# Kernel optimization log

Measured on AMD Instinct MI355X. Metric: run time of the kernel, lower is better.

The kernel has to match this reference:

```python
import jax, jax.numpy as jnp
import numpy as np

BANDWIDTH = 0.1
N_STEPS = 5
TOL = 1e-3
BASE = 3
COORD_OFFSET = 512   # bins assumed within (-512, 511] per dim
COORD_BITS = 10      # 3 dims * 10 bits = 30 bits, fits int32


def _generate_offsets(d, base=3):
    # replicates torch.meshgrid(indexing='ij') over arange(-1, base-1)
    ranges = [np.arange(-1, base - 1) for _ in range(d)]
    mesh = np.meshgrid(*ranges, indexing='ij')
    return jnp.asarray(np.stack(mesh, axis=-1).reshape(-1, d), dtype=jnp.int32)


def _pack_keys(bins):
    # bins: (..., d) int32 -> unique scalar int32 key per bin coordinate
    d = bins.shape[-1]
    key = jnp.zeros(bins.shape[:-1], dtype=jnp.int32)
    for k in range(d):  # tiny fixed loop over dims
        key = (key << COORD_BITS) | (bins[..., k] + COORD_OFFSET)
    return key


def _step(X, offsets, bandwidth):
    # One mean-shift step: bin points, scatter-add sums/counts over the
    # union of offset-shifted bins (torch.unique replaced by exact key
    # packing + sort-based grouping, fixed shapes for jit).
    n, d = X.shape
    m = offsets.shape[0]  # base ** d
    bins = (X / bandwidth).astype(jnp.int32)          # trunc-toward-zero == torch .int()
    shifted = bins[:, None, :] + offsets[None, :, :]  # (n, m, d)
    keys = _pack_keys(shifted).reshape(-1)            # (n*m,)
    K = keys.shape[0]

    order = jnp.argsort(keys)
    skeys = keys[order]
    new_grp = jnp.concatenate(
        [jnp.zeros((1,), jnp.int32), (skeys[1:] != skeys[:-1]).astype(jnp.int32)]
    )
    seg = jnp.cumsum(new_grp)                         # group id per sorted position

    # X repeated once per offset (matches X.repeat(1, m).reshape(-1, d))
    Xflat = jnp.broadcast_to(X[:, None, :], (n, m, d)).reshape(-1, d)
    sum_per = jax.ops.segment_sum(Xflat[order], seg, num_segments=K)          # (K, d)
    cnt_per = jax.ops.segment_sum(jnp.ones((K,), X.dtype), seg, num_segments=K)

    # segment id per original (unsorted) flat position == inverse_indices
    seg_orig = jnp.zeros((K,), seg.dtype).at[order].set(seg)
    sum_mapped = sum_per[seg_orig].reshape(n, m, d).sum(axis=1)   # (n, d)
    cnt_mapped = cnt_per[seg_orig].reshape(n, m).sum(axis=1)      # (n,)
    return sum_mapped / cnt_mapped[:, None]


def setup_inputs() -> dict:
    key = jax.random.key(0)
    X = jax.random.normal(key, (200000, 3), dtype=jnp.float32)
    return {"X": X}


def reference(X):
    n, d = X.shape
    offsets = _generate_offsets(d, BASE)

    def body(carry, _):
        Xc, done = carry
        Xn = _step(Xc, offsets, BANDWIDTH)
        Xn = jnp.where(done, Xc, Xn)  # freeze once converged (== early break)
        conv = jnp.max(jnp.linalg.norm(Xn - Xc, axis=1)) <= TOL
        return (Xn, done | conv), None

    (Xout, _), _ = jax.lax.scan(body, (X, jnp.array(False)), None, length=N_STEPS)
    return Xout
```

## Files before the change

kernel.cpp:

```cpp
#include <hip/hip_runtime.h>


constexpr float BW   = 0.1f;
constexpr float TOL2 = 1e-6f;
constexpr int DIM  = 112, OFF = 56;
constexpr int DIM2 = DIM * DIM;
constexpr int CELLS = DIM * DIM * DIM;
constexpr int CLW = CELLS / 32;
constexpr int RDIM = 16, RC = 7;
constexpr int NREG = RDIM * RDIM * RDIM;
constexpr int RC3 = RC * RC * RC;
constexpr int NB_A = 128, BLK = 256;
constexpr int NF = 2048;
constexpr int IPB = 51;
constexpr float FPS = 16777216.0f;
constexpr double FPSI = 1.0 / 16777216.0;

typedef float vf2 __attribute__((ext_vector_type(2)));

__device__ __forceinline__ int clampb(int v) { return v < 0 ? 0 : (v > DIM - 1 ? DIM - 1 : v); }
__device__ __forceinline__ int binf(float v) { return clampb((int)(v / BW) + OFF); }
__device__ __forceinline__ int flatb(int bx, int by, int bz) { return (bx * DIM + by) * DIM + bz; }
__device__ __forceinline__ int regOf(int bx, int by, int bz) {
    return ((bx / RC) * RDIM + (by / RC)) * RDIM + (bz / RC);
}
__device__ __forceinline__ int lcOf(int bx, int by, int bz) {
    return ((bx % RC) * RC + (by % RC)) * RC + (bz % RC);
}

__device__ __forceinline__ void pk_add(float* p, float a, float b) {
#if defined(__has_builtin) && __has_builtin(__builtin_amdgcn_global_atomic_fadd_v2f32)
    vf2 v = {a, b};
    __builtin_amdgcn_global_atomic_fadd_v2f32((vf2*)p, v);
#else
    atomicAdd(p, a);
    atomicAdd(p + 1, b);
#endif
}

__launch_bounds__(BLK)
__global__ void k_histA(const float* __restrict__ X, int n, int* __restrict__ blockHist,
                        float4* __restrict__ zeroA, float4* __restrict__ zeroB) {
    __shared__ int h[NREG];
    for (int i = threadIdx.x; i < NREG; i += blockDim.x) h[i] = 0;
    __syncthreads();
    int stride = gridDim.x * blockDim.x;
    for (int i = blockIdx.x * blockDim.x + threadIdx.x; i < n; i += stride) {
        float x = X[3 * i + 0], y = X[3 * i + 1], z = X[3 * i + 2];
        atomicAdd(&h[regOf(binf(x), binf(y), binf(z))], 1);
    }
    __syncthreads();
    for (int i = threadIdx.x; i < NREG; i += blockDim.x)
        blockHist[blockIdx.x * NREG + i] = h[i];
    for (int i = blockIdx.x * blockDim.x + threadIdx.x; i < CELLS; i += stride) {
        zeroA[i] = make_float4(0.f, 0.f, 0.f, 0.f);
        zeroB[i] = make_float4(0.f, 0.f, 0.f, 0.f);
    }
}

__global__ void k_colscan(int* __restrict__ blockHist, int* __restrict__ regionPS) {
    int r = blockIdx.x * blockDim.x + threadIdx.x;
    if (r >= NREG) return;
    int run = 0;
    for (int b = 0; b < NB_A; ++b) {
        int idx = b * NREG + r;
        int v = blockHist[idx];
        blockHist[idx] = run;
        run += v;
    }
    regionPS[r] = run;
}

__launch_bounds__(1024)
__global__ void k_regprefix(int* __restrict__ regionPS) {
    __shared__ int buf[1024];
    int t = threadIdx.x;
    int v0 = regionPS[4 * t + 0], v1 = regionPS[4 * t + 1];
    int v2 = regionPS[4 * t + 2], v3 = regionPS[4 * t + 3];
    int s = v0 + v1 + v2 + v3;
    buf[t] = s;
    __syncthreads();
    for (int d = 1; d < 1024; d <<= 1) {
        int add = (t >= d) ? buf[t - d] : 0;
        __syncthreads();
        buf[t] += add;
        __syncthreads();
    }
    int excl = buf[t] - s;
    regionPS[4 * t + 0] = excl;
    regionPS[4 * t + 1] = excl + v0;
    regionPS[4 * t + 2] = excl + v0 + v1;
    regionPS[4 * t + 3] = excl + v0 + v1 + v2;
    if (t == 1023) regionPS[4096] = buf[1023];
}

__launch_bounds__(BLK)
__global__ void k_scatterA(const float* __restrict__ X, int n,
                           const int* __restrict__ blockHist,
                           const int* __restrict__ regionPS,
                           float4* __restrict__ bucket, float4* __restrict__ zeroC) {
    __shared__ int cur[NREG];
    for (int i = threadIdx.x; i < NREG; i += blockDim.x) cur[i] = 0;
    __syncthreads();
    int stride = gridDim.x * blockDim.x;
    for (int i = blockIdx.x * blockDim.x + threadIdx.x; i < n; i += stride) {
        float x = X[3 * i + 0], y = X[3 * i + 1], z = X[3 * i + 2];
        int r = regOf(binf(x), binf(y), binf(z));
        int pos = regionPS[r] + blockHist[blockIdx.x * NREG + r] + atomicAdd(&cur[r], 1);
        bucket[pos] = make_float4(x, y, z, __int_as_float(i));
    }
    for (int i = blockIdx.x * blockDim.x + threadIdx.x; i < CELLS; i += stride)
        zeroC[i] = make_float4(0.f, 0.f, 0.f, 0.f);
}

__launch_bounds__(BLK)
__global__ void k_binB(const float4* __restrict__ bucket, const int* __restrict__ regionPS,
                       float4* __restrict__ A, int* __restrict__ E0,
                       int* __restrict__ PIdx, int* __restrict__ gM0) {
    __shared__ unsigned long long aX[RC3], aY[RC3], aZ[RC3];
    __shared__ unsigned aC[RC3];
    __shared__ int cidx[RC3];
    __shared__ int cnt, cur, sBase;
    int r = blockIdx.x;
    for (int c = threadIdx.x; c < RC3; c += blockDim.x) {
        aX[c] = 0ull; aY[c] = 0ull; aZ[c] = 0ull; aC[c] = 0u;
    }
    if (threadIdx.x == 0) { cnt = 0; cur = 0; }
    __syncthreads();
    int start = regionPS[r], end = regionPS[r + 1];
    for (int i = start + threadIdx.x; i < end; i += blockDim.x) {
        float4 p = bucket[i];
        int lc = lcOf(binf(p.x), binf(p.y), binf(p.z));
        atomicAdd(&aX[lc], (unsigned long long)(long long)rintf(p.x * FPS));
        atomicAdd(&aY[lc], (unsigned long long)(long long)rintf(p.y * FPS));
        atomicAdd(&aZ[lc], (unsigned long long)(long long)rintf(p.z * FPS));
        atomicAdd(&aC[lc], 1u);
    }
    __syncthreads();
    int myc = 0;
    for (int c = threadIdx.x; c < RC3; c += blockDim.x)
        if (aC[c] > 0u) ++myc;
    if (myc) atomicAdd(&cnt, myc);
    __syncthreads();
    if (threadIdx.x == 0 && cnt > 0) sBase = atomicAdd(gM0, cnt);
    __syncthreads();
    int rx = r / (RDIM * RDIM), ry = (r / RDIM) % RDIM, rz = r % RDIM;
    for (int c = threadIdx.x; c < RC3; c += blockDim.x) {
        if (aC[c] > 0u) {
            int idx = sBase + atomicAdd(&cur, 1);
            cidx[c] = idx;
            int bx = rx * RC + c / (RC * RC);
            int by = ry * RC + (c / RC) % RC;
            int bz = rz * RC + c % RC;
            int b = flatb(bx, by, bz);
            E0[idx] = b;
            A[b] = make_float4((float)((double)(long long)aX[c] * FPSI),
                               (float)((double)(long long)aY[c] * FPSI),
                               (float)((double)(long long)aZ[c] * FPSI),
                               (float)aC[c]);
        }
    }
    __syncthreads();
    for (int i = start + threadIdx.x; i < end; i += blockDim.x) {
        float4 p = bucket[i];
        int lc = lcOf(binf(p.x), binf(p.y), binf(p.z));
        PIdx[__float_as_int(p.w)] = cidx[lc];
    }
}

__launch_bounds__(BLK)
__global__ void k_fused(
    const float4* __restrict__ src, const int* __restrict__ list, const int* __restrict__ pK,
    float4* __restrict__ REo, int* __restrict__ IDXo, float4* __restrict__ eposInit,
    float4* __restrict__ tgt, unsigned* __restrict__ clT,
    int updS, const float* __restrict__ X, int n, const int* __restrict__ PIdx,
    const float4* __restrict__ REp, const int* __restrict__ IDXp,
    const int* __restrict__ pM0, float4* __restrict__ epos,
    unsigned* __restrict__ notConv,
    const int* __restrict__ clearList, const int* __restrict__ pKc,
    float4* __restrict__ clearGrid, int chkMask, int lastStep) {
    __shared__ float4 sh[BLK];
    __shared__ float shW[IPB];
    __shared__ unsigned sFlag;
    if (threadIdx.x == 0) sFlag = 0;
    __syncthreads();
    int K = *pK;
    int NC = (K + IPB - 1) / IPB;
    int BC = NC;
    if (BC > NF - 256) BC = NF - 256;
    const float t5[5] = {1.f, 2.f, 3.f, 2.f, 1.f};
    bool moved = false;

    if ((int)blockIdx.x < BC) {
        bool frozen = false;
        if (chkMask) {
            #pragma unroll
            for (int t = 1; t <= 4; ++t)
                if ((chkMask >> t) & 1) frozen |= (notConv[t] == 0u);
        }
        if (!frozen) {
        int first, last, step;
        if (BC >= 64) {
            int xcd = blockIdx.x & 7, loc = blockIdx.x >> 3;
            int cpx = (NC + 7) >> 3;
            int bpx = ((BC - 1 - xcd) >> 3) + 1;
            first = xcd * cpx + loc;
            last = (xcd + 1) * cpx; if (last > NC) last = NC;
            step = bpx;
        } else {
            first = blockIdx.x; last = NC; step = BC;
        }
        for (int ib = first; ib < last; ib += step) {
            int li = threadIdx.x / 5;
            int dx = threadIdx.x % 5;
            int item = ib * IPB + li;
            float4 part = make_float4(0.f, 0.f, 0.f, 0.f);
            if (li < IPB && item < K) {
                int b = list[item];
                int bx = b / DIM2, rem = b % DIM2;
                int by = rem / DIM, bz = rem % DIM;
                if (dx == 2) shW[li] = src[b].w;
                int ix = bx + dx - 2;
                if ((unsigned)ix < (unsigned)DIM) {
                    float wx = t5[dx];
                    if (by >= 2 && by <= DIM - 3 && bz >= 2 && bz <= DIM - 3) {
                        #pragma unroll
                        for (int dy = 0; dy < 5; ++dy) {
                            float wxy = wx * t5[dy];
                            const float4* row = src + flatb(ix, by + dy - 2, bz - 2);
                            #pragma unroll
                            for (int dz = 0; dz < 5; ++dz) {
                                float w = wxy * t5[dz];
                                float4 e = row[dz];
                                part.x = fmaf(w, e.x, part.x);
                                part.y = fmaf(w, e.y, part.y);
                                part.z = fmaf(w, e.z, part.z);
                                part.w = fmaf(w, e.w, part.w);
                            }
                        }
                    } else {
                        for (int dy = 0; dy < 5; ++dy) {
                            int iy = by + dy - 2;
                            if ((unsigned)iy >= (unsigned)DIM) continue;
                            float wxy = wx * t5[dy];
                            for (int dz = 0; dz < 5; ++dz) {
                                int iz = bz + dz - 2;
                                if ((unsigned)iz >= (unsigned)DIM) continue;
                                float w = wxy * t5[dz];
                                float4 e = src[flatb(ix, iy, iz)];
                                part.x = fmaf(w, e.x, part.x);
                                part.y = fmaf(w, e.y, part.y);
                                part.z = fmaf(w, e.z, part.z);
                                part.w = fmaf(w, e.w, part.w);
                            }
                        }
                    }
                }
            }
            sh[threadIdx.x] = part;
            __syncthreads();
            if (threadIdx.x < 64) {
                int item2 = ib * IPB + threadIdx.x;
                bool valid = (threadIdx.x < IPB) && (item2 < K);
                int bn = -1;
                float4 sv = make_float4(0.f, 0.f, 0.f, 0.f);
                if (valid) {
                    int base5 = threadIdx.x * 5;
                    float4 a0 = sh[base5 + 0], a1 = sh[base5 + 1], a2 = sh[base5 + 2];
                    float4 a3 = sh[base5 + 3], a4 = sh[base5 + 4];
                    float sx = a0.x + a1.x + a2.x + a3.x + a4.x;
                    float sy = a0.y + a1.y + a2.y + a3.y + a4.y;
                    float sz = a0.z + a1.z + a2.z + a3.z + a4.z;
                    float sc = a0.w + a1.w + a2.w + a3.w + a4.w;
                    int b = list[item2];
                    float W = shW[threadIdx.x];
                    float4 np = make_float4(sx / sc, sy / sc, sz / sc, W);
                    REo[item2] = np;
                    IDXo[b] = item2;
                    if (eposInit) eposInit[item2] = np;
                    if (!lastStep) {
                        bn = flatb(binf(np.x), binf(np.y), binf(np.z));
                        sv = make_float4(W * np.x, W * np.y, W * np.z, W);
                    }
                }
                if (!lastStep) {
                    int pbn = __shfl_up(bn, 1, 64);
                    unsigned f = (threadIdx.x == 0 || pbn != bn) ? 1u : 0u;
                    unsigned nf = __shfl_down(f, 1, 64);
                    bool leader = valid && (threadIdx.x == 63 || nf != 0u);
                    #pragma unroll
                    for (int off = 1; off < 64; off <<= 1) {
                        float ox = __shfl_up(sv.x, off, 64);
                        float oy = __shfl_up(sv.y, off, 64);
                        float oz = __shfl_up(sv.z, off, 64);
                        float ow = __shfl_up(sv.w, off, 64);
                        unsigned of = __shfl_up(f, off, 64);
                        if ((int)threadIdx.x >= off) {
                            if (!f) { sv.x += ox; sv.y += oy; sv.z += oz; sv.w += ow; }
                            f |= of;
                        }
                    }
                    if (leader) {
                        float* cell = (float*)&tgt[bn];
                        pk_add(cell + 0, sv.x, sv.y);
                        pk_add(cell + 2, sv.z, sv.w);
                        atomicOr(&clT[(unsigned)bn >> 5], 1u << (bn & 31));
                    }
                }
            }
            __syncthreads();
        }
        }
    } else {
        int U = (updS > 0) ? (X ? n : *pM0) : 0;
        int CL = clearList ? *pKc : 0;
        int total = U + CL;
        bool done = false;
        if (updS > 1) {
            for (int t = 1; t < updS; ++t) done |= (notConv[t] == 0u);
        }
        int stride = (NF - BC) * blockDim.x;
        for (int idx = (blockIdx.x - BC) * blockDim.x + threadIdx.x; idx < total;
             idx += stride) {
            if (idx < U) {
                int e = idx;
                if (X) {
                    float x = X[3 * e + 0], y = X[3 * e + 1], z = X[3 * e + 2];
                    float4 rr = REp[PIdx[e]];
                    float ex = rr.x - x, ey = rr.y - y, ez = rr.z - z;
                    moved |= (fmaf(ex, ex, fmaf(ey, ey, ez * ez)) > TOL2);
                } else if (!done) {
                    float4 p = epos[e];
                    int j = IDXp[flatb(binf(p.x), binf(p.y), binf(p.z))];
                    float4 rr = REp[j];
                    float ex = rr.x - p.x, ey = rr.y - p.y, ez = rr.z - p.z;
                    moved |= (fmaf(ex, ex, fmaf(ey, ey, ez * ez)) > TOL2);
                    epos[e] = make_float4(rr.x, rr.y, rr.z, p.w);
                }
            } else {
                clearGrid[clearList[idx - U]] = make_float4(0.f, 0.f, 0.f, 0.f);
            }
        }
    }
    if (moved) sFlag = 1;
    __syncthreads();
    if (threadIdx.x == 0 && updS > 0 && sFlag) notConv[updS] = 1u;
}

__launch_bounds__(BLK)
__global__ void k_compactM(unsigned* __restrict__ mask, int* __restrict__ listOut,
                           int* __restrict__ pKout) {
    __shared__ int scan[BLK];
    __shared__ int sBase;
    int i = blockIdx.x * blockDim.x + threadIdx.x;
    unsigned w = (i < CLW) ? mask[i] : 0u;
    if (i < CLW && w) mask[i] = 0u;
    int c = __popc(w);
    scan[threadIdx.x] = c;
    __syncthreads();
    for (int d = 1; d < BLK; d <<= 1) {
        int add = (threadIdx.x >= (unsigned)d) ? scan[threadIdx.x - d] : 0;
        __syncthreads();
        scan[threadIdx.x] += add;
        __syncthreads();
    }
    if (threadIdx.x == BLK - 1) {
        int tot = scan[BLK - 1];
        sBase = tot ? atomicAdd(pKout, tot) : 0;
    }
    __syncthreads();
    int base = sBase + scan[threadIdx.x] - c;
    int bb = i * 32;
    while (w) {
        int b = __ffs(w) - 1;
        listOut[base++] = bb + b;
        w &= w - 1;
    }
}

__launch_bounds__(BLK)
__global__ void k_fin(const float4* __restrict__ REa, const int* __restrict__ IDXa,
                      const float4* __restrict__ epos, const int* __restrict__ pM0,
                      const unsigned* __restrict__ notConv, float4* __restrict__ fpos) {
    int M0 = *pM0;
    bool done = false;
    for (int t = 1; t <= 4; ++t) done |= (notConv[t] == 0u);
    for (int e = blockIdx.x * blockDim.x + threadIdx.x; e < M0;
         e += gridDim.x * blockDim.x) {
        float4 p = epos[e];
        if (!done) {
            float4 rr = REa[IDXa[flatb(binf(p.x), binf(p.y), binf(p.z))]];
            p.x = rr.x; p.y = rr.y; p.z = rr.z;
        }
        fpos[e] = p;
    }
}

__global__ void k_map(const int* __restrict__ PIdx, int n, const float4* __restrict__ fpos,
                      float* __restrict__ out) {
    int i = blockIdx.x * blockDim.x + threadIdx.x;
    if (i >= n) return;
    float4 p = fpos[PIdx[i]];
    out[3 * i + 0] = p.x;
    out[3 * i + 1] = p.y;
    out[3 * i + 2] = p.z;
}

extern "C" void kernel_launch(void* const* d_in, const int* in_sizes, int n_in,
                              void* d_out, int out_size, void* d_ws, size_t ws_size,
                              hipStream_t stream) {
    const float* X = (const float*)d_in[0];
    int n = in_sizes[0] / 3;

    char* ws = (char*)d_ws;
    int*      cnt     = (int*)ws;
    unsigned* notConv = (unsigned*)(ws + 32);
    size_t mB = (size_t)CLW * 4;
    size_t gB = (size_t)CELLS * 16;
    unsigned* m0 = (unsigned*)(ws + 256);
    unsigned* m1 = (unsigned*)(ws + 256 + mB);
    float4* A = (float4*)(ws + 256 + 2 * mB);
    float4* B = (float4*)((char*)A + gB);
    float4* C = (float4*)((char*)B + gB);
    int* IDXa = (int*)((char*)C + gB);
    int* IDXb = IDXa + CELLS;
    float4* REa  = (float4*)(IDXb + CELLS);
    float4* REb  = REa + n;
    float4* epos = REb + n;
    int* E0   = (int*)(epos + n);
    int* La   = E0 + n;
    int* Lb   = La + n;
    int* Lc   = Lb + n;
    int* Ld   = Lc + n;
    int* PIdx = Ld + n;
    float4* bucket = (float4*)(PIdx + n);
    int* blockHist = (int*)(bucket + n);
    int* regionPS  = blockHist + NB_A * NREG;

    hipMemsetAsync(ws, 0, 256 + 2 * mB, stream);

    const int NCM = (CLW + BLK - 1) / BLK;

    k_histA<<<NB_A, BLK, 0, stream>>>(X, n, blockHist, A, B);
    k_colscan<<<NREG / BLK, BLK, 0, stream>>>(blockHist, regionPS);
    k_regprefix<<<1, 1024, 0, stream>>>(regionPS);
    k_scatterA<<<NB_A, BLK, 0, stream>>>(X, n, blockHist, regionPS, bucket, C);
    k_binB<<<NREG, BLK, 0, stream>>>(bucket, regionPS, A, E0, PIdx, &cnt[1]);

    k_fused<<<NF, BLK, 0, stream>>>(A, E0, &cnt[1], REa, IDXa, epos,
                                    B, m0,
                                    0, nullptr, n, nullptr, nullptr, nullptr, nullptr,
                                    nullptr, notConv, nullptr, nullptr, nullptr, 0, 0);
    k_compactM<<<NCM, BLK, 0, stream>>>(m0, La, &cnt[2]);
    k_fused<<<NF, BLK, 0, stream>>>(B, La, &cnt[2], REb, IDXb, nullptr,
                                    C, m1,
                                    1, X, n, PIdx, REa, IDXa, &cnt[1], nullptr,
                                    notConv, E0, &cnt[1], A, 0, 0);
    k_compactM<<<NCM, BLK, 0, stream>>>(m1, Lb, &cnt[3]);
    k_fused<<<NF, BLK, 0, stream>>>(C, Lb, &cnt[3], REa, IDXa, nullptr,
                                    A, m0,
                                    2, nullptr, n, nullptr, REb, IDXb, &cnt[1], epos,
                                    notConv, La, &cnt[2], B, 0b00010, 0);
    k_compactM<<<NCM, BLK, 0, stream>>>(m0, Lc, &cnt[4]);
    k_fused<<<NF, BLK, 0, stream>>>(A, Lc, &cnt[4], REb, IDXb, nullptr,
                                    B, m1,
                                    3, nullptr, n, nullptr, REa, IDXa, &cnt[1], epos,
                                    notConv, nullptr, nullptr, nullptr, 0b00110, 0);
    k_compactM<<<NCM, BLK, 0, stream>>>(m1, Ld, &cnt[5]);
    k_fused<<<NF, BLK, 0, stream>>>(B, Ld, &cnt[5], REa, IDXa, nullptr,
                                    nullptr, nullptr,
                                    4, nullptr, n, nullptr, REb, IDXb, &cnt[1], epos,
                                    notConv, nullptr, nullptr, nullptr, 0b01110, 1);

    k_fin<<<256, BLK, 0, stream>>>(REa, IDXa, epos, &cnt[1], notConv, REb);
    k_map<<<(n + BLK - 1) / BLK, BLK, 0, stream>>>(PIdx, n, REb, (float*)d_out);
}
```

Before: 246.8 us.

## Gather stencil neighbors through compact index grid instead of dense float4 grid

The dense float4 grid reads in the 5x5x5 stencil are replaced by reads of an int index grid. Each index is validated against the compact list, and only then is the neighbor's float4 loaded from a compacted array. The compaction kernel now also writes that index grid and copies the grid values into the compact array. The goal is to cut memory traffic from mostly-empty cells, at the cost of an extra dependent load per neighbor and divergent validation branches. The stale-index validation also replaces the old grid clearing for some steps, and changes which buffers are cleared.

```diff
diff --git a/kernel.cpp b/kernel.cpp
--- a/kernel.cpp
+++ b/kernel.cpp
@@ -115,7 +115,8 @@
 
 __launch_bounds__(BLK)
 __global__ void k_binB(const float4* __restrict__ bucket, const int* __restrict__ regionPS,
-                       float4* __restrict__ A, int* __restrict__ E0,
+                       float4* __restrict__ AC, int* __restrict__ E0,
+                       int* __restrict__ IDXa,
                        int* __restrict__ PIdx, int* __restrict__ gM0) {
     __shared__ unsigned long long aX[RC3], aY[RC3], aZ[RC3];
     __shared__ unsigned aC[RC3];
@@ -154,10 +155,11 @@
             int bz = rz * RC + c % RC;
             int b = flatb(bx, by, bz);
             E0[idx] = b;
-            A[b] = make_float4((float)((double)(long long)aX[c] * FPSI),
-                               (float)((double)(long long)aY[c] * FPSI),
-                               (float)((double)(long long)aZ[c] * FPSI),
-                               (float)aC[c]);
+            IDXa[b] = idx;
+            AC[idx] = make_float4((float)((double)(long long)aX[c] * FPSI),
+                                  (float)((double)(long long)aY[c] * FPSI),
+                                  (float)((double)(long long)aZ[c] * FPSI),
+                                  (float)aC[c]);
         }
     }
     __syncthreads();
@@ -170,8 +172,9 @@
 
 __launch_bounds__(BLK)
 __global__ void k_fused(
-    const float4* __restrict__ src, const int* __restrict__ list, const int* __restrict__ pK,
-    float4* __restrict__ REo, int* __restrict__ IDXo, float4* __restrict__ eposInit,
+    const float4* __restrict__ AC, const int* __restrict__ list, const int* __restrict__ pK,
+    const int* __restrict__ IDXsrc,
+    float4* __restrict__ REo, float4* __restrict__ eposInit,
     float4* __restrict__ tgt, unsigned* __restrict__ clT,
     int updS, const float* __restrict__ X, int n, const int* __restrict__ PIdx,
     const float4* __restrict__ REp, const int* __restrict__ IDXp,
@@ -180,7 +183,6 @@
     const int* __restrict__ clearList, const int* __restrict__ pKc,
     float4* __restrict__ clearGrid, int chkMask, int lastStep) {
     __shared__ float4 sh[BLK];
-    __shared__ float shW[IPB];
     __shared__ unsigned sFlag;
     if (threadIdx.x == 0) sFlag = 0;
     __syncthreads();
@@ -219,23 +221,34 @@
                 int b = list[item];
                 int bx = b / DIM2, rem = b % DIM2;
                 int by = rem / DIM, bz = rem % DIM;
-                if (dx == 2) shW[li] = src[b].w;
                 int ix = bx + dx - 2;
                 if ((unsigned)ix < (unsigned)DIM) {
                     float wx = t5[dx];
                     if (by >= 2 && by <= DIM - 3 && bz >= 2 && bz <= DIM - 3) {
+                        int idxv[25];
+                        #pragma unroll
+                        for (int dy = 0; dy < 5; ++dy) {
+                            const int* gr = IDXsrc + flatb(ix, by + dy - 2, bz - 2);
+                            #pragma unroll
+                            for (int dz = 0; dz < 5; ++dz)
+                                idxv[dy * 5 + dz] = gr[dz];
+                        }
+                        int rowb = flatb(ix, by - 2, bz - 2);
                         #pragma unroll
                         for (int dy = 0; dy < 5; ++dy) {
                             float wxy = wx * t5[dy];
-                            const float4* row = src + flatb(ix, by + dy - 2, bz - 2);
                             #pragma unroll
                             for (int dz = 0; dz < 5; ++dz) {
-                                float w = wxy * t5[dz];
-                                float4 e = row[dz];
-                                part.x = fmaf(w, e.x, part.x);
-                                part.y = fmaf(w, e.y, part.y);
-                                part.z = fmaf(w, e.z, part.z);
-                                part.w = fmaf(w, e.w, part.w);
+                                int id = idxv[dy * 5 + dz];
+                                if ((unsigned)id < (unsigned)K &&
+                                    list[id] == rowb + dy * DIM + dz) {
+                                    float4 e = AC[id];
+                                    float w = wxy * t5[dz];
+                                    part.x = fmaf(w, e.x, part.x);
+                                    part.y = fmaf(w, e.y, part.y);
+                                    part.z = fmaf(w, e.z, part.z);
+                                    part.w = fmaf(w, e.w, part.w);
+                                }
                             }
                         }
                     } else {
@@ -246,12 +259,16 @@
                             for (int dz = 0; dz < 5; ++dz) {
                                 int iz = bz + dz - 2;
                                 if ((unsigned)iz >= (unsigned)DIM) continue;
-                                float w = wxy * t5[dz];
-                                float4 e = src[flatb(ix, iy, iz)];
-                                part.x = fmaf(w, e.x, part.x);
-                                part.y = fmaf(w, e.y, part.y);
-                                part.z = fmaf(w, e.z, part.z);
-                                part.w = fmaf(w, e.w, part.w);
+                                int cell = flatb(ix, iy, iz);
+                                int id = IDXsrc[cell];
+                                if ((unsigned)id < (unsigned)K && list[id] == cell) {
+                                    float4 e = AC[id];
+                                    float w = wxy * t5[dz];
+                                    part.x = fmaf(w, e.x, part.x);
+                                    part.y = fmaf(w, e.y, part.y);
+                                    part.z = fmaf(w, e.z, part.z);
+                                    part.w = fmaf(w, e.w, part.w);
+                                }
                             }
                         }
                     }
@@ -272,11 +289,9 @@
                     float sy = a0.y + a1.y + a2.y + a3.y + a4.y;
                     float sz = a0.z + a1.z + a2.z + a3.z + a4.z;
                     float sc = a0.w + a1.w + a2.w + a3.w + a4.w;
-                    int b = list[item2];
-                    float W = shW[threadIdx.x];
+                    float W = AC[item2].w;
                     float4 np = make_float4(sx / sc, sy / sc, sz / sc, W);
                     REo[item2] = np;
-                    IDXo[b] = item2;
                     if (eposInit) eposInit[item2] = np;
                     if (!lastStep) {
                         bn = flatb(binf(np.x), binf(np.y), binf(np.z));
@@ -348,8 +363,9 @@
 }
 
 __launch_bounds__(BLK)
-__global__ void k_compactM(unsigned* __restrict__ mask, int* __restrict__ listOut,
-                           int* __restrict__ pKout) {
+__global__ void k_compactM(unsigned* __restrict__ mask, const float4* __restrict__ G,
+                           int* __restrict__ listOut, int* __restrict__ pKout,
+                           int* __restrict__ IDXout, float4* __restrict__ ACout) {
     __shared__ int scan[BLK];
     __shared__ int sBase;
     int i = blockIdx.x * blockDim.x + threadIdx.x;
@@ -373,7 +389,11 @@
     int bb = i * 32;
     while (w) {
         int b = __ffs(w) - 1;
-        listOut[base++] = bb + b;
+        int cell = bb + b;
+        listOut[base] = cell;
+        IDXout[cell] = base;
+        ACout[base] = G[cell];
+        ++base;
         w &= w - 1;
     }
 }
@@ -436,6 +456,7 @@
     float4* bucket = (float4*)(PIdx + n);
     int* blockHist = (int*)(bucket + n);
     int* regionPS  = blockHist + NB_A * NREG;
+    float4* AC = (float4*)(regionPS + 4104);
 
     hipMemsetAsync(ws, 0, 256 + 2 * mB, stream);
 
@@ -445,29 +466,29 @@
     k_colscan<<<NREG / BLK, BLK, 0, stream>>>(blockHist, regionPS);
     k_regprefix<<<1, 1024, 0, stream>>>(regionPS);
     k_scatterA<<<NB_A, BLK, 0, stream>>>(X, n, blockHist, regionPS, bucket, C);
-    k_binB<<<NREG, BLK, 0, stream>>>(bucket, regionPS, A, E0, PIdx, &cnt[1]);
-
-    k_fused<<<NF, BLK, 0, stream>>>(A, E0, &cnt[1], REa, IDXa, epos,
+    k_binB<<<NREG, BLK, 0, stream>>>(bucket, regionPS, AC, E0, IDXa, PIdx, &cnt[1]);
+
+    k_fused<<<NF, BLK, 0, stream>>>(AC, E0, &cnt[1], IDXa, REa, epos,
                                     B, m0,
                                     0, nullptr, n, nullptr, nullptr, nullptr, nullptr,
                                     nullptr, notConv, nullptr, nullptr, nullptr, 0, 0);
-    k_compactM<<<NCM, BLK, 0, stream>>>(m0, La, &cnt[2]);
-    k_fused<<<NF, BLK, 0, stream>>>(B, La, &cnt[2], REb, IDXb, nullptr,
+    k_compactM<<<NCM, BLK, 0, stream>>>(m0, B, La, &cnt[2], IDXb, AC);
+    k_fused<<<NF, BLK, 0, stream>>>(AC, La, &cnt[2], IDXb, REb, nullptr,
                                     C, m1,
-                                    1, X, n, PIdx, REa, IDXa, &cnt[1], nullptr,
-                                    notConv, E0, &cnt[1], A, 0, 0);
-    k_compactM<<<NCM, BLK, 0, stream>>>(m1, Lb, &cnt[3]);
-    k_fused<<<NF, BLK, 0, stream>>>(C, Lb, &cnt[3], REa, IDXa, nullptr,
+                                    1, X, n, PIdx, REa, nullptr, &cnt[1], nullptr,
+                                    notConv, nullptr, nullptr, nullptr, 0, 0);
+    k_compactM<<<NCM, BLK, 0, stream>>>(m1, C, Lb, &cnt[3], IDXa, AC);
+    k_fused<<<NF, BLK, 0, stream>>>(AC, Lb, &cnt[3], IDXa, REa, nullptr,
                                     A, m0,
                                     2, nullptr, n, nullptr, REb, IDXb, &cnt[1], epos,
                                     notConv, La, &cnt[2], B, 0b00010, 0);
-    k_compactM<<<NCM, BLK, 0, stream>>>(m0, Lc, &cnt[4]);
-    k_fused<<<NF, BLK, 0, stream>>>(A, Lc, &cnt[4], REb, IDXb, nullptr,
+    k_compactM<<<NCM, BLK, 0, stream>>>(m0, A, Lc, &cnt[4], IDXb, AC);
+    k_fused<<<NF, BLK, 0, stream>>>(AC, Lc, &cnt[4], IDXb, REb, nullptr,
                                     B, m1,
                                     3, nullptr, n, nullptr, REa, IDXa, &cnt[1], epos,
                                     notConv, nullptr, nullptr, nullptr, 0b00110, 0);
-    k_compactM<<<NCM, BLK, 0, stream>>>(m1, Ld, &cnt[5]);
-    k_fused<<<NF, BLK, 0, stream>>>(B, Ld, &cnt[5], REa, IDXa, nullptr,
+    k_compactM<<<NCM, BLK, 0, stream>>>(m1, B, Ld, &cnt[5], IDXa, AC);
+    k_fused<<<NF, BLK, 0, stream>>>(AC, Ld, &cnt[5], IDXa, REa, nullptr,
                                     nullptr, nullptr,
                                     4, nullptr, n, nullptr, REb, IDXb, &cnt[1], epos,
                                     notConv, nullptr, nullptr, nullptr, 0b01110, 1);
```

Result: slower. 313.4 us (+27.0%).
